# Kernel tuning notes

Hardware: AMD Instinct MI355X
Metric: run time of the kernel (lower is better)

Reference implementation:

```python
import jax, jax.numpy as jnp
import numpy as np

N, E, F, H, O, R = 50000, 600000, 128, 128, 64, 8


def setup_inputs() -> dict:
    key = jax.random.key(0)
    ks = jax.random.split(key, 10)
    x = jax.random.normal(ks[0], (N, F), dtype=jnp.float32)
    edge_index = jax.random.randint(ks[1], (2, E), 0, N, dtype=jnp.int64)
    edge_weight = jax.random.uniform(ks[2], (E,), dtype=jnp.float32)
    edge_type = jax.random.randint(ks[3], (E,), 0, R, dtype=jnp.int64)
    s = 1.0 / np.sqrt(F)
    W1 = jax.random.uniform(ks[4], (R, F, H), jnp.float32, -s, s)
    root1 = jax.random.uniform(ks[5], (F, H), jnp.float32, -s, s)
    bias1 = jnp.zeros((H,), jnp.float32)
    sh = 1.0 / np.sqrt(H)
    W2 = jax.random.uniform(ks[6], (R, H, O), jnp.float32, -sh, sh)
    root2 = jax.random.uniform(ks[7], (H, O), jnp.float32, -sh, sh)
    bias2 = jnp.zeros((O,), jnp.float32)
    return {"x": x, "edge_index": edge_index, "edge_weight": edge_weight,
            "edge_type": edge_type, "W1": W1, "root1": root1, "bias1": bias1,
            "W2": W2, "root2": root2, "bias2": bias2}


def _rgcn_conv(x, src, dst, et, ew, W, root, bias, num_nodes):
    # project every node by every relation: [N, R, out] (cheaper than per-edge
    # materialization of weight[edge_type] which is E x in x out)
    proj = jnp.einsum('nd,rdo->nro', x, W)
    # per-edge message = x_j @ W[edge_type] * edge_weight  -> [E, out]
    msg = proj[src, et] * ew[:, None]
    # weighted scatter-mean over destination nodes
    agg = jax.ops.segment_sum(msg, dst, num_segments=num_nodes)
    cnt = jax.ops.segment_sum(jnp.ones_like(ew), dst, num_segments=num_nodes)
    agg = agg / jnp.maximum(cnt, 1.0)[:, None]
    # root (self) transform + bias
    return agg + x @ root + bias


def reference(x, edge_index, edge_weight, edge_type, W1, root1, bias1, W2, root2, bias2):
    src, dst = edge_index[0], edge_index[1]
    et = edge_type.astype(jnp.int32)
    # min-max normalize edge weights as in RGCN.forward
    ew = (edge_weight - edge_weight.min()) / (edge_weight.max() - edge_weight.min() + 1e-8)
    n = x.shape[0]
    h = jax.nn.relu(_rgcn_conv(x, src, dst, et, ew, W1, root1, bias1, n))
    return _rgcn_conv(h, src, dst, et, ew, W2, root2, bias2, n)
```

## Files before the change

kernel.cpp:

```cpp
#include <hip/hip_runtime.h>

#define F_DIM 128
#define H_DIM 128
#define O_DIM 64
#define R_NUM 8

typedef __attribute__((ext_vector_type(8))) short bf16x8;
typedef __attribute__((ext_vector_type(4))) float f32x4;
typedef __attribute__((ext_vector_type(8))) unsigned short u16x8;

union V8 { bf16x8 v; short4 h[2]; };

__device__ __forceinline__ unsigned short f2b(float f) {
    unsigned u = __float_as_uint(f);
    u += 0x7FFFu + ((u >> 16) & 1u);
    return (unsigned short)(u >> 16);
}
__device__ __forceinline__ float b2f(unsigned short b) {
    return __uint_as_float(((unsigned)b) << 16);
}

__global__ __launch_bounds__(256) void setupA(
    const float* __restrict__ ew, const int* __restrict__ dst,
    const int* __restrict__ et, int E, int* __restrict__ deg2,
    float* __restrict__ bmn, float* __restrict__ bmx,
    const float* __restrict__ x, unsigned short* __restrict__ xb, long x4,
    const float* __restrict__ W1, const float* __restrict__ root1,
    const float* __restrict__ W2, const float* __restrict__ root2,
    unsigned short* __restrict__ wt1, unsigned short* __restrict__ wt2) {
    __shared__ float smn[256], smx[256];
    const int tid = threadIdx.x;
    const int gstride = gridDim.x * blockDim.x;
    int g0 = blockIdx.x * blockDim.x + tid;

    float mn = 1e30f, mx = -1e30f;
    for (int i = g0; i < E; i += gstride) {
        atomicAdd(&deg2[dst[i] * R_NUM + et[i]], 1);
        float v = ew[i];
        mn = fminf(mn, v);
        mx = fmaxf(mx, v);
    }
    smn[tid] = mn; smx[tid] = mx;
    __syncthreads();
    for (int s = 128; s > 0; s >>= 1) {
        if (tid < s) {
            smn[tid] = fminf(smn[tid], smn[tid + s]);
            smx[tid] = fmaxf(smx[tid], smx[tid + s]);
        }
        __syncthreads();
    }
    if (tid == 0) { bmn[blockIdx.x] = smn[0]; bmx[blockIdx.x] = smx[0]; }

    for (long i = g0; i < x4; i += gstride) {
        float4 v = ((const float4*)x)[i];
        ushort4 o;
        o.x = f2b(v.x); o.y = f2b(v.y); o.z = f2b(v.z); o.w = f2b(v.w);
        ((ushort4*)xb)[i] = o;
    }

    const int n1 = 9 * 128 * 128, n2 = 9 * 64 * 128;
    for (int idx = g0; idx < n1 + n2; idx += gstride) {
        if (idx < n1) {
            int r = idx / (128 * 128), rem = idx % (128 * 128);
            int n = rem / 128, k = rem % 128;
            float v = (r < 8) ? W1[((size_t)r * 128 + k) * 128 + n]
                              : root1[(size_t)k * 128 + n];
            wt1[idx] = f2b(v);
        } else {
            int j = idx - n1;
            int r = j / (64 * 128), rem = j % (64 * 128);
            int n = rem / 128, k = rem % 128;
            float v = (r < 8) ? W2[((size_t)r * 128 + k) * 64 + n]
                              : root2[(size_t)k * 64 + n];
            wt2[j] = f2b(v);
        }
    }
}

__global__ void scan1_kernel(const int* __restrict__ deg, int* __restrict__ rp,
                             int* __restrict__ bsum, float* __restrict__ invc,
                             int M, int N) {
    __shared__ int s[256];
    int base = blockIdx.x * 2048;
    int t = threadIdx.x;
    int v[8]; int loc = 0;
#pragma unroll
    for (int i = 0; i < 8; ++i) {
        int idx = base + t * 8 + i;
        v[i] = (idx < M) ? deg[idx] : 0;
        loc += v[i];
    }
    int node = blockIdx.x * 256 + t;
    if (node < N) invc[node] = 1.0f / (float)max(loc, 1);
    s[t] = loc;
    __syncthreads();
    for (int off = 1; off < 256; off <<= 1) {
        int x = (t >= off) ? s[t - off] : 0;
        __syncthreads();
        s[t] += x;
        __syncthreads();
    }
    int run = s[t] - loc;
#pragma unroll
    for (int i = 0; i < 8; ++i) {
        int idx = base + t * 8 + i;
        if (idx < M) rp[idx] = run;
        run += v[i];
    }
    if (t == 255) bsum[blockIdx.x] = s[255];
}

__global__ void scan2_mm(int* bsum, int nb, const float* __restrict__ bmn,
                         const float* __restrict__ bmx, float* mm) {
    __shared__ int s[256];
    __shared__ float smn[256], smx[256];
    int t = threadIdx.x;
    int v = (t < nb) ? bsum[t] : 0;
    s[t] = v;
    smn[t] = fminf(bmn[t], bmn[t + 256]);
    smx[t] = fmaxf(bmx[t], bmx[t + 256]);
    __syncthreads();
    for (int off = 1; off < 256; off <<= 1) {
        int x = (t >= off) ? s[t - off] : 0;
        __syncthreads();
        s[t] += x;
        __syncthreads();
    }
    if (t < nb) bsum[t] = s[t] - v;
    for (int r = 128; r > 0; r >>= 1) {
        if (t < r) {
            smn[t] = fminf(smn[t], smn[t + r]);
            smx[t] = fmaxf(smx[t], smx[t + r]);
        }
        __syncthreads();
    }
    if (t == 0) { mm[0] = smn[0]; mm[1] = smx[0]; }
}

__global__ void scan3_kernel(int* __restrict__ rp, const int* __restrict__ bsum, int M) {
    int i = blockIdx.x * blockDim.x + threadIdx.x;
    if (i < M) rp[i] += bsum[i >> 11];
}

__global__ void fill2_kernel(const int* __restrict__ src, const int* __restrict__ dst,
                             const int* __restrict__ et, const float* __restrict__ ew,
                             const float* __restrict__ mm, const float* __restrict__ invc,
                             int* __restrict__ rp2, unsigned* __restrict__ erec, int E) {
    int e = blockIdx.x * blockDim.x + threadIdx.x;
    if (e >= E) return;
    int d = dst[e];
    int pos = atomicAdd(&rp2[d * R_NUM + et[e]], 1);
    float mn = mm[0], mx = mm[1];
    unsigned wq = f2b((ew[e] - mn) / (mx - mn + 1e-8f) * invc[d]);
    erec[pos] = (wq << 17) | (unsigned)src[e];
}

__global__ __launch_bounds__(256) void gather_y(
    const int* __restrict__ rp2, const unsigned* __restrict__ erec,
    const unsigned short* __restrict__ inp,
    unsigned short* __restrict__ y, int N) {
    int gid = blockIdx.x * 256 + threadIdx.x;
    int seg = gid >> 4;
    int n = seg >> 3;
    if (n >= N) return;
    int j = (gid & 15) * 8;
    int beg = (seg == 0) ? 0 : rp2[seg - 1];
    int end = rp2[seg];
    float acc[8] = {0.f, 0.f, 0.f, 0.f, 0.f, 0.f, 0.f, 0.f};
    int k = beg;
    for (; k + 2 <= end; k += 2) {
        unsigned r0 = erec[k], r1 = erec[k + 1];
        float w0 = __uint_as_float((r0 >> 1) & 0x7FFF8000u);
        float w1 = __uint_as_float((r1 >> 1) & 0x7FFF8000u);
        u16x8 v0 = *(const u16x8*)(inp + (size_t)(r0 & 0x1FFFFu) * 128 + j);
        u16x8 v1 = *(const u16x8*)(inp + (size_t)(r1 & 0x1FFFFu) * 128 + j);
#pragma unroll
        for (int c = 0; c < 8; ++c) acc[c] += w0 * b2f(v0[c]);
#pragma unroll
        for (int c = 0; c < 8; ++c) acc[c] += w1 * b2f(v1[c]);
    }
    if (k < end) {
        unsigned r0 = erec[k];
        float w0 = __uint_as_float((r0 >> 1) & 0x7FFF8000u);
        u16x8 v0 = *(const u16x8*)(inp + (size_t)(r0 & 0x1FFFFu) * 128 + j);
#pragma unroll
        for (int c = 0; c < 8; ++c) acc[c] += w0 * b2f(v0[c]);
    }
    u16x8 o;
#pragma unroll
    for (int c = 0; c < 8; ++c) o[c] = f2b(acc[c]);
    *(u16x8*)(y + (size_t)seg * 128 + j) = o;
}

template <int NCOL, bool RELU, bool OUTB>
__global__ __launch_bounds__(256) void gemm_y(
    const unsigned short* __restrict__ y,
    const unsigned short* __restrict__ inp,
    const unsigned short* __restrict__ Wt,
    const float* __restrict__ bias,
    unsigned short* __restrict__ outb, float* __restrict__ outf, int N)
{
    constexpr int NT = NCOL / 16;
    __shared__ unsigned short smem[64 * 132 + NCOL * 132];
    unsigned short* ys  = smem;
    unsigned short* wsd = smem + 64 * 132;

    const int tid = threadIdx.x;
    const int w = tid >> 6, lane = tid & 63;
    const int quad = lane >> 4, l15 = lane & 15;
    const int n0 = blockIdx.x * 64;

    f32x4 acc[NT];
#pragma unroll
    for (int nt = 0; nt < NT; ++nt) acc[nt] = (f32x4){0.f, 0.f, 0.f, 0.f};

    for (int r = 0; r < 9; ++r) {
#pragma unroll
        for (int it = 0; it < NCOL / 16; ++it) {
            int u = tid + it * 256;
            int row = u >> 4, seg = u & 15;
            V8 v;
            v.v = *(const bf16x8*)(Wt + ((size_t)r * NCOL + row) * 128 + seg * 8);
            *(short4*)&wsd[row * 132 + seg * 8]     = v.h[0];
            *(short4*)&wsd[row * 132 + seg * 8 + 4] = v.h[1];
        }
#pragma unroll
        for (int it = 0; it < 4; ++it) {
            int u = tid + it * 256;
            int row = u >> 4, seg = u & 15;
            int node = n0 + row;
            if (node >= N) node = N - 1;
            const unsigned short* src = (r < 8)
                ? y + ((size_t)node * R_NUM + r) * 128 + seg * 8
                : inp + (size_t)node * 128 + seg * 8;
            V8 v; v.v = *(const bf16x8*)src;
            *(short4*)&ys[row * 132 + seg * 8]     = v.h[0];
            *(short4*)&ys[row * 132 + seg * 8 + 4] = v.h[1];
        }
        __syncthreads();
        const unsigned short* yrow = ys + (size_t)(w * 16 + l15) * 132 + quad * 8;
#pragma unroll
        for (int k2 = 0; k2 < 4; ++k2) {
            V8 b;
            b.h[0] = *(const short4*)(yrow + k2 * 32);
            b.h[1] = *(const short4*)(yrow + k2 * 32 + 4);
#pragma unroll
            for (int nt = 0; nt < NT; ++nt) {
                const unsigned short* ar = wsd + (size_t)(nt * 16 + l15) * 132
                                           + k2 * 32 + quad * 8;
                V8 av;
                av.h[0] = *(const short4*)ar;
                av.h[1] = *(const short4*)(ar + 4);
                acc[nt] = __builtin_amdgcn_mfma_f32_16x16x32_bf16(av.v, b.v, acc[nt], 0, 0, 0);
            }
        }
        __syncthreads();
    }

    const int gn = tid >> 2, gq = tid & 3;
    const int gnode = n0 + gn;
    if (OUTB) {
        unsigned short* stg = smem;
#pragma unroll
        for (int nt = 0; nt < NT; ++nt) {
            int c0 = nt * 16 + quad * 4;
            float4 bs = *(const float4*)(bias + c0);
            float v0 = acc[nt][0] + bs.x, v1 = acc[nt][1] + bs.y;
            float v2 = acc[nt][2] + bs.z, v3 = acc[nt][3] + bs.w;
            if (RELU) {
                v0 = fmaxf(v0, 0.f); v1 = fmaxf(v1, 0.f);
                v2 = fmaxf(v2, 0.f); v3 = fmaxf(v3, 0.f);
            }
            short4 o;
            o.x = (short)f2b(v0); o.y = (short)f2b(v1);
            o.z = (short)f2b(v2); o.w = (short)f2b(v3);
            *(short4*)&stg[(w * 16 + l15) * 136 + c0] = o;
        }
        __syncthreads();
        if (gnode < N) {
            const unsigned short* srow = stg + gn * 136 + gq * (NCOL / 4);
            unsigned short* drow = outb + (size_t)gnode * NCOL + gq * (NCOL / 4);
#pragma unroll
            for (int c = 0; c < NCOL / 32; ++c)
                *(bf16x8*)(drow + c * 8) = *(const bf16x8*)(srow + c * 8);
        }
    } else {
        float* stg = (float*)smem;
#pragma unroll
        for (int nt = 0; nt < NT; ++nt) {
            int c0 = nt * 16 + quad * 4;
            float4 bs = *(const float4*)(bias + c0);
            float v0 = acc[nt][0] + bs.x, v1 = acc[nt][1] + bs.y;
            float v2 = acc[nt][2] + bs.z, v3 = acc[nt][3] + bs.w;
            if (RELU) {
                v0 = fmaxf(v0, 0.f); v1 = fmaxf(v1, 0.f);
                v2 = fmaxf(v2, 0.f); v3 = fmaxf(v3, 0.f);
            }
            *(float4*)&stg[(w * 16 + l15) * 68 + c0] = make_float4(v0, v1, v2, v3);
        }
        __syncthreads();
        if (gnode < N) {
            const float* srow = stg + gn * 68 + gq * (NCOL / 4);
            float* drow = outf + (size_t)gnode * NCOL + gq * (NCOL / 4);
#pragma unroll
            for (int c = 0; c < NCOL / 16; ++c)
                *(float4*)(drow + c * 4) = *(const float4*)(srow + c * 4);
        }
    }
}

extern "C" void kernel_launch(void* const* d_in, const int* in_sizes, int n_in,
                              void* d_out, int out_size, void* d_ws, size_t ws_size,
                              hipStream_t stream) {
    const float* x     = (const float*)d_in[0];
    const int*   ei    = (const int*)d_in[1];
    const float* ew    = (const float*)d_in[2];
    const int*   et    = (const int*)d_in[3];
    const float* W1    = (const float*)d_in[4];
    const float* root1 = (const float*)d_in[5];
    const float* bias1 = (const float*)d_in[6];
    const float* W2    = (const float*)d_in[7];
    const float* root2 = (const float*)d_in[8];
    const float* bias2 = (const float*)d_in[9];

    const int N = in_sizes[0] / F_DIM;
    const int E = in_sizes[2];
    const int M2 = N * R_NUM;
    const int* srcp = ei;
    const int* dstp = ei + E;

    int* base = (int*)d_ws;
    float* mm    = (float*)base;
    float* invc  = (float*)(base + 16);
    int*   deg2  = base + 16 + N;
    int*   rp2   = deg2 + M2;
    int*   bsum  = rp2 + M2;
    float* bmn   = (float*)(bsum + 256);
    float* bmx   = bmn + 512;
    unsigned* erec = (unsigned*)(bmx + 512);
    unsigned short* xb  = (unsigned short*)(erec + E);
    unsigned short* hb  = xb + (size_t)N * 128;
    unsigned short* wt1 = hb + (size_t)N * 128;
    unsigned short* wt2 = wt1 + 9 * 128 * 128;
    unsigned short* y   = wt2 + 9 * 64 * 128;

    const int TB = 256;
    int blocksE = (E + TB - 1) / TB;
    int nb = (M2 + 2047) / 2048;
    long x4 = (long)N * 128 / 4;

    hipMemsetAsync(deg2, 0, (size_t)M2 * sizeof(int), stream);
    setupA<<<512, TB, 0, stream>>>(ew, dstp, et, E, deg2, bmn, bmx,
                                   x, xb, x4, W1, root1, W2, root2, wt1, wt2);
    scan1_kernel<<<nb, TB, 0, stream>>>(deg2, rp2, bsum, invc, M2, N);
    scan2_mm<<<1, TB, 0, stream>>>(bsum, nb, bmn, bmx, mm);
    scan3_kernel<<<(M2 + TB - 1) / TB, TB, 0, stream>>>(rp2, bsum, M2);
    fill2_kernel<<<blocksE, TB, 0, stream>>>(srcp, dstp, et, ew, mm, invc,
                                             rp2, erec, E);

    int gatB = (int)(((long)M2 * 16 + TB - 1) / TB);
    int gB = (N + 63) / 64;

    gather_y<<<gatB, TB, 0, stream>>>(rp2, erec, xb, y, N);
    gemm_y<H_DIM, true, true><<<gB, TB, 0, stream>>>(y, xb, wt1, bias1, hb, nullptr, N);
    gather_y<<<gatB, TB, 0, stream>>>(rp2, erec, hb, y, N);
    gemm_y<O_DIM, false, false><<<gB, TB, 0, stream>>>(y, hb, wt2, bias2, nullptr,
                                                       (float*)d_out, N);
}
```

Baseline: 317.5 us.

## Double-buffer Y tiles and keep weight fragments in registers in gemm_y

Rewrites the gemm_y inner loop so each wave owns a slice of output columns and loads its weight fragments directly from global memory into registers, dropping the per-relation LDS staging of the weight matrix. Y tiles are double-buffered in LDS, with the next relation's tile prefetched into registers during the MFMAs, leaving one barrier per iteration instead of two. This aims to overlap global loads with compute and cut LDS traffic and syncs, at the cost of more VGPRs for weight fragments and uncoalesced-ish global weight reads, which may lower occupancy.

Result: slower. 325.3 us (+2.5%).

```diff
diff --git a/kernel.cpp b/kernel.cpp
--- a/kernel.cpp
+++ b/kernel.cpp
@@ -200,58 +200,79 @@
     const float* __restrict__ bias,
     unsigned short* __restrict__ outb, float* __restrict__ outf, int N)
 {
-    constexpr int NT = NCOL / 16;
-    __shared__ unsigned short smem[64 * 132 + NCOL * 132];
-    unsigned short* ys  = smem;
-    unsigned short* wsd = smem + 64 * 132;
+    constexpr int NTW = NCOL / 64;
+    __shared__ unsigned short ybuf[2][64 * 132];
 
     const int tid = threadIdx.x;
     const int w = tid >> 6, lane = tid & 63;
     const int quad = lane >> 4, l15 = lane & 15;
     const int n0 = blockIdx.x * 64;
 
-    f32x4 acc[NT];
-#pragma unroll
-    for (int nt = 0; nt < NT; ++nt) acc[nt] = (f32x4){0.f, 0.f, 0.f, 0.f};
+    const int srow = tid >> 4;
+    const int sseg = tid & 15;
+
+    f32x4 acc[4][NTW];
+#pragma unroll
+    for (int m = 0; m < 4; ++m)
+#pragma unroll
+        for (int nt = 0; nt < NTW; ++nt) acc[m][nt] = (f32x4){0.f, 0.f, 0.f, 0.f};
+
+#pragma unroll
+    for (int it = 0; it < 4; ++it) {
+        int row = srow + it * 16;
+        int node = n0 + row;
+        if (node >= N) node = N - 1;
+        V8 v;
+        v.v = *(const bf16x8*)(y + ((size_t)node * R_NUM + 0) * 128 + sseg * 8);
+        *(short4*)&ybuf[0][row * 132 + sseg * 8]     = v.h[0];
+        *(short4*)&ybuf[0][row * 132 + sseg * 8 + 4] = v.h[1];
+    }
+    __syncthreads();
 
     for (int r = 0; r < 9; ++r) {
-#pragma unroll
-        for (int it = 0; it < NCOL / 16; ++it) {
-            int u = tid + it * 256;
-            int row = u >> 4, seg = u & 15;
-            V8 v;
-            v.v = *(const bf16x8*)(Wt + ((size_t)r * NCOL + row) * 128 + seg * 8);
-            *(short4*)&wsd[row * 132 + seg * 8]     = v.h[0];
-            *(short4*)&wsd[row * 132 + seg * 8 + 4] = v.h[1];
-        }
-#pragma unroll
-        for (int it = 0; it < 4; ++it) {
-            int u = tid + it * 256;
-            int row = u >> 4, seg = u & 15;
-            int node = n0 + row;
-            if (node >= N) node = N - 1;
-            const unsigned short* src = (r < 8)
-                ? y + ((size_t)node * R_NUM + r) * 128 + seg * 8
-                : inp + (size_t)node * 128 + seg * 8;
-            V8 v; v.v = *(const bf16x8*)src;
-            *(short4*)&ys[row * 132 + seg * 8]     = v.h[0];
-            *(short4*)&ys[row * 132 + seg * 8 + 4] = v.h[1];
-        }
-        __syncthreads();
-        const unsigned short* yrow = ys + (size_t)(w * 16 + l15) * 132 + quad * 8;
-#pragma unroll
-        for (int k2 = 0; k2 < 4; ++k2) {
-            V8 b;
-            b.h[0] = *(const short4*)(yrow + k2 * 32);
-            b.h[1] = *(const short4*)(yrow + k2 * 32 + 4);
-#pragma unroll
-            for (int nt = 0; nt < NT; ++nt) {
-                const unsigned short* ar = wsd + (size_t)(nt * 16 + l15) * 132
-                                           + k2 * 32 + quad * 8;
-                V8 av;
-                av.h[0] = *(const short4*)ar;
-                av.h[1] = *(const short4*)(ar + 4);
-                acc[nt] = __builtin_amdgcn_mfma_f32_16x16x32_bf16(av.v, b.v, acc[nt], 0, 0, 0);
+        const int buf = r & 1;
+        V8 pre[4];
+        if (r < 8) {
+            const int rn = r + 1;
+#pragma unroll
+            for (int it = 0; it < 4; ++it) {
+                int row = srow + it * 16;
+                int node = n0 + row;
+                if (node >= N) node = N - 1;
+                const unsigned short* src = (rn < 8)
+                    ? y + ((size_t)node * R_NUM + rn) * 128 + sseg * 8
+                    : inp + (size_t)node * 128 + sseg * 8;
+                pre[it].v = *(const bf16x8*)src;
+            }
+        }
+        bf16x8 afr[NTW][4];
+#pragma unroll
+        for (int nt = 0; nt < NTW; ++nt)
+#pragma unroll
+            for (int k2 = 0; k2 < 4; ++k2)
+                afr[nt][k2] = *(const bf16x8*)(
+                    Wt + ((size_t)r * NCOL + (w * NTW + nt) * 16 + l15) * 128
+                       + k2 * 32 + quad * 8);
+#pragma unroll
+        for (int m = 0; m < 4; ++m) {
+            const unsigned short* yrow = &ybuf[buf][(m * 16 + l15) * 132 + quad * 8];
+#pragma unroll
+            for (int k2 = 0; k2 < 4; ++k2) {
+                V8 b;
+                b.h[0] = *(const short4*)(yrow + k2 * 32);
+                b.h[1] = *(const short4*)(yrow + k2 * 32 + 4);
+#pragma unroll
+                for (int nt = 0; nt < NTW; ++nt)
+                    acc[m][nt] = __builtin_amdgcn_mfma_f32_16x16x32_bf16(
+                        afr[nt][k2], b.v, acc[m][nt], 0, 0, 0);
+            }
+        }
+        if (r < 8) {
+#pragma unroll
+            for (int it = 0; it < 4; ++it) {
+                int row = srow + it * 16;
+                *(short4*)&ybuf[buf ^ 1][row * 132 + sseg * 8]     = pre[it].h[0];
+                *(short4*)&ybuf[buf ^ 1][row * 132 + sseg * 8 + 4] = pre[it].h[1];
             }
         }
         __syncthreads();
@@ -260,51 +281,57 @@
     const int gn = tid >> 2, gq = tid & 3;
     const int gnode = n0 + gn;
     if (OUTB) {
-        unsigned short* stg = smem;
-#pragma unroll
-        for (int nt = 0; nt < NT; ++nt) {
-            int c0 = nt * 16 + quad * 4;
-            float4 bs = *(const float4*)(bias + c0);
-            float v0 = acc[nt][0] + bs.x, v1 = acc[nt][1] + bs.y;
-            float v2 = acc[nt][2] + bs.z, v3 = acc[nt][3] + bs.w;
-            if (RELU) {
-                v0 = fmaxf(v0, 0.f); v1 = fmaxf(v1, 0.f);
-                v2 = fmaxf(v2, 0.f); v3 = fmaxf(v3, 0.f);
-            }
-            short4 o;
-            o.x = (short)f2b(v0); o.y = (short)f2b(v1);
-            o.z = (short)f2b(v2); o.w = (short)f2b(v3);
-            *(short4*)&stg[(w * 16 + l15) * 136 + c0] = o;
-        }
+        unsigned short* stg = &ybuf[0][0];
+#pragma unroll
+        for (int m = 0; m < 4; ++m)
+#pragma unroll
+            for (int nt = 0; nt < NTW; ++nt) {
+                int node_l = m * 16 + l15;
+                int c0 = (w * NTW + nt) * 16 + quad * 4;
+                float4 bs = *(const float4*)(bias + c0);
+                float v0 = acc[m][nt][0] + bs.x, v1 = acc[m][nt][1] + bs.y;
+                float v2 = acc[m][nt][2] + bs.z, v3 = acc[m][nt][3] + bs.w;
+                if (RELU) {
+                    v0 = fmaxf(v0, 0.f); v1 = fmaxf(v1, 0.f);
+                    v2 = fmaxf(v2, 0.f); v3 = fmaxf(v3, 0.f);
+                }
+                short4 o;
+                o.x = (short)f2b(v0); o.y = (short)f2b(v1);
+                o.z = (short)f2b(v2); o.w = (short)f2b(v3);
+                *(short4*)&stg[node_l * 136 + c0] = o;
+            }
         __syncthreads();
         if (gnode < N) {
-            const unsigned short* srow = stg + gn * 136 + gq * (NCOL / 4);
+            const unsigned short* srw = stg + gn * 136 + gq * (NCOL / 4);
             unsigned short* drow = outb + (size_t)gnode * NCOL + gq * (NCOL / 4);
 #pragma unroll
             for (int c = 0; c < NCOL / 32; ++c)
-                *(bf16x8*)(drow + c * 8) = *(const bf16x8*)(srow + c * 8);
+                *(bf16x8*)(drow + c * 8) = *(const bf16x8*)(srw + c * 8);
         }
     } else {
-        float* stg = (float*)smem;
-#pragma unroll
-        for (int nt = 0; nt < NT; ++nt) {
-            int c0 = nt * 16 + quad * 4;
-            float4 bs = *(const float4*)(bias + c0);
-            float v0 = acc[nt][0] + bs.x, v1 = acc[nt][1] + bs.y;
-            float v2 = acc[nt][2] + bs.z, v3 = acc[nt][3] + bs.w;
-            if (RELU) {
-                v0 = fmaxf(v0, 0.f); v1 = fmaxf(v1, 0.f);
-                v2 = fmaxf(v2, 0.f); v3 = fmaxf(v3, 0.f);
-            }
-            *(float4*)&stg[(w * 16 + l15) * 68 + c0] = make_float4(v0, v1, v2, v3);
-        }
+        float* stg = (float*)&ybuf[0][0];
+#pragma unroll
+        for (int m = 0; m < 4; ++m)
+#pragma unroll
+            for (int nt = 0; nt < NTW; ++nt) {
+                int node_l = m * 16 + l15;
+                int c0 = (w * NTW + nt) * 16 + quad * 4;
+                float4 bs = *(const float4*)(bias + c0);
+                float v0 = acc[m][nt][0] + bs.x, v1 = acc[m][nt][1] + bs.y;
+                float v2 = acc[m][nt][2] + bs.z, v3 = acc[m][nt][3] + bs.w;
+                if (RELU) {
+                    v0 = fmaxf(v0, 0.f); v1 = fmaxf(v1, 0.f);
+                    v2 = fmaxf(v2, 0.f); v3 = fmaxf(v3, 0.f);
+                }
+                *(float4*)&stg[node_l * 68 + c0] = make_float4(v0, v1, v2, v3);
+            }
         __syncthreads();
         if (gnode < N) {
-            const float* srow = stg + gn * 68 + gq * (NCOL / 4);
+            const float* srw = stg + gn * 68 + gq * (NCOL / 4);
             float* drow = outf + (size_t)gnode * NCOL + gq * (NCOL / 4);
 #pragma unroll
             for (int c = 0; c < NCOL / 16; ++c)
-                *(float4*)(drow + c * 4) = *(const float4*)(srow + c * 4);
+                *(float4*)(drow + c * 4) = *(const float4*)(srw + c * 4);
         }
     }
 }
```

## Project layer-2 features before aggregation and fold scan offsets into consumers

Applied to the files above, without the earlier changes.

Layer 2 now projects every node by every relation (and root) into a 64-wide bf16 buffer first, then gathers the projected rows per destination node. Because the output width is 64 rather than 128, this halves the bytes moved in the second edge gather, and it drops the separate aggregate-then-GEMM path for that layer. It also removes the scan3 pass by adding the block prefix sums inside fill2 and the gather kernels. The cost is a larger intermediate (9×N×64) and a per-relation serial loop in the final gather.

New measurement: 298.2 us. 1.06x faster.

```diff
diff --git a/kernel.cpp b/kernel.cpp
--- a/kernel.cpp
+++ b/kernel.cpp
@@ -137,26 +137,24 @@
     if (t == 0) { mm[0] = smn[0]; mm[1] = smx[0]; }
 }
 
-__global__ void scan3_kernel(int* __restrict__ rp, const int* __restrict__ bsum, int M) {
-    int i = blockIdx.x * blockDim.x + threadIdx.x;
-    if (i < M) rp[i] += bsum[i >> 11];
-}
-
 __global__ void fill2_kernel(const int* __restrict__ src, const int* __restrict__ dst,
                              const int* __restrict__ et, const float* __restrict__ ew,
                              const float* __restrict__ mm, const float* __restrict__ invc,
-                             int* __restrict__ rp2, unsigned* __restrict__ erec, int E) {
+                             int* __restrict__ rp2, const int* __restrict__ bsum,
+                             unsigned* __restrict__ erec, int E) {
     int e = blockIdx.x * blockDim.x + threadIdx.x;
     if (e >= E) return;
     int d = dst[e];
-    int pos = atomicAdd(&rp2[d * R_NUM + et[e]], 1);
+    int i = d * R_NUM + et[e];
+    int pos = atomicAdd(&rp2[i], 1) + bsum[i >> 11];
     float mn = mm[0], mx = mm[1];
     unsigned wq = f2b((ew[e] - mn) / (mx - mn + 1e-8f) * invc[d]);
     erec[pos] = (wq << 17) | (unsigned)src[e];
 }
 
 __global__ __launch_bounds__(256) void gather_y(
-    const int* __restrict__ rp2, const unsigned* __restrict__ erec,
+    const int* __restrict__ rp2, const int* __restrict__ bsum,
+    const unsigned* __restrict__ erec,
     const unsigned short* __restrict__ inp,
     unsigned short* __restrict__ y, int N) {
     int gid = blockIdx.x * 256 + threadIdx.x;
@@ -164,8 +162,8 @@
     int n = seg >> 3;
     if (n >= N) return;
     int j = (gid & 15) * 8;
-    int beg = (seg == 0) ? 0 : rp2[seg - 1];
-    int end = rp2[seg];
+    int beg = (seg == 0) ? 0 : rp2[seg - 1] + bsum[(seg - 1) >> 11];
+    int end = rp2[seg] + bsum[seg >> 11];
     float acc[8] = {0.f, 0.f, 0.f, 0.f, 0.f, 0.f, 0.f, 0.f};
     int k = beg;
     for (; k + 2 <= end; k += 2) {
@@ -192,13 +190,13 @@
     *(u16x8*)(y + (size_t)seg * 128 + j) = o;
 }
 
-template <int NCOL, bool RELU, bool OUTB>
+template <int NCOL, bool RELU>
 __global__ __launch_bounds__(256) void gemm_y(
     const unsigned short* __restrict__ y,
     const unsigned short* __restrict__ inp,
     const unsigned short* __restrict__ Wt,
     const float* __restrict__ bias,
-    unsigned short* __restrict__ outb, float* __restrict__ outf, int N)
+    unsigned short* __restrict__ outb, int N)
 {
     constexpr int NT = NCOL / 16;
     __shared__ unsigned short smem[64 * 132 + NCOL * 132];
@@ -259,54 +257,156 @@
 
     const int gn = tid >> 2, gq = tid & 3;
     const int gnode = n0 + gn;
-    if (OUTB) {
-        unsigned short* stg = smem;
-#pragma unroll
-        for (int nt = 0; nt < NT; ++nt) {
+    unsigned short* stg = smem;
+#pragma unroll
+    for (int nt = 0; nt < NT; ++nt) {
+        int c0 = nt * 16 + quad * 4;
+        float4 bs = *(const float4*)(bias + c0);
+        float v0 = acc[nt][0] + bs.x, v1 = acc[nt][1] + bs.y;
+        float v2 = acc[nt][2] + bs.z, v3 = acc[nt][3] + bs.w;
+        if (RELU) {
+            v0 = fmaxf(v0, 0.f); v1 = fmaxf(v1, 0.f);
+            v2 = fmaxf(v2, 0.f); v3 = fmaxf(v3, 0.f);
+        }
+        short4 o;
+        o.x = (short)f2b(v0); o.y = (short)f2b(v1);
+        o.z = (short)f2b(v2); o.w = (short)f2b(v3);
+        *(short4*)&stg[(w * 16 + l15) * 136 + c0] = o;
+    }
+    __syncthreads();
+    if (gnode < N) {
+        const unsigned short* srw = stg + gn * 136 + gq * (NCOL / 4);
+        unsigned short* drow = outb + (size_t)gnode * NCOL + gq * (NCOL / 4);
+#pragma unroll
+        for (int c = 0; c < NCOL / 32; ++c)
+            *(bf16x8*)(drow + c * 8) = *(const bf16x8*)(srw + c * 8);
+    }
+}
+
+__global__ __launch_bounds__(256) void gemm_proj2(
+    const unsigned short* __restrict__ h,
+    const unsigned short* __restrict__ Wt,
+    unsigned short* __restrict__ proj2,
+    int N)
+{
+    __shared__ unsigned short hs[64 * 132];
+    __shared__ unsigned short wsd[64 * 132];
+    __shared__ unsigned short ts[64 * 68];
+
+    const int tid = threadIdx.x;
+    const int w = tid >> 6, lane = tid & 63;
+    const int quad = lane >> 4, l15 = lane & 15;
+    const int n0 = blockIdx.x * 64;
+
+#pragma unroll
+    for (int it = 0; it < 4; ++it) {
+        int u = tid + it * 256;
+        int row = u >> 4, seg = u & 15;
+        int node = n0 + row;
+        if (node >= N) node = N - 1;
+        V8 v; v.v = *(const bf16x8*)(h + (size_t)node * 128 + seg * 8);
+        *(short4*)&hs[row * 132 + seg * 8]     = v.h[0];
+        *(short4*)&hs[row * 132 + seg * 8 + 4] = v.h[1];
+    }
+
+    for (int r = 0; r < 9; ++r) {
+#pragma unroll
+        for (int it = 0; it < 4; ++it) {
+            int u = tid + it * 256;
+            int row = u >> 4, seg = u & 15;
+            V8 v;
+            v.v = *(const bf16x8*)(Wt + ((size_t)r * 64 + row) * 128 + seg * 8);
+            *(short4*)&wsd[row * 132 + seg * 8]     = v.h[0];
+            *(short4*)&wsd[row * 132 + seg * 8 + 4] = v.h[1];
+        }
+        __syncthreads();
+        f32x4 acc[4];
+#pragma unroll
+        for (int nt = 0; nt < 4; ++nt) acc[nt] = (f32x4){0.f, 0.f, 0.f, 0.f};
+        const unsigned short* yrow = hs + (size_t)(w * 16 + l15) * 132 + quad * 8;
+#pragma unroll
+        for (int k2 = 0; k2 < 4; ++k2) {
+            V8 b;
+            b.h[0] = *(const short4*)(yrow + k2 * 32);
+            b.h[1] = *(const short4*)(yrow + k2 * 32 + 4);
+#pragma unroll
+            for (int nt = 0; nt < 4; ++nt) {
+                const unsigned short* ar = wsd + (size_t)(nt * 16 + l15) * 132
+                                           + k2 * 32 + quad * 8;
+                V8 av;
+                av.h[0] = *(const short4*)ar;
+                av.h[1] = *(const short4*)(ar + 4);
+                acc[nt] = __builtin_amdgcn_mfma_f32_16x16x32_bf16(av.v, b.v, acc[nt], 0, 0, 0);
+            }
+        }
+        unsigned short* tw = ts + w * 16 * 68;
+#pragma unroll
+        for (int nt = 0; nt < 4; ++nt) {
             int c0 = nt * 16 + quad * 4;
-            float4 bs = *(const float4*)(bias + c0);
-            float v0 = acc[nt][0] + bs.x, v1 = acc[nt][1] + bs.y;
-            float v2 = acc[nt][2] + bs.z, v3 = acc[nt][3] + bs.w;
-            if (RELU) {
-                v0 = fmaxf(v0, 0.f); v1 = fmaxf(v1, 0.f);
-                v2 = fmaxf(v2, 0.f); v3 = fmaxf(v3, 0.f);
-            }
             short4 o;
-            o.x = (short)f2b(v0); o.y = (short)f2b(v1);
-            o.z = (short)f2b(v2); o.w = (short)f2b(v3);
-            *(short4*)&stg[(w * 16 + l15) * 136 + c0] = o;
-        }
-        __syncthreads();
-        if (gnode < N) {
-            const unsigned short* srow = stg + gn * 136 + gq * (NCOL / 4);
-            unsigned short* drow = outb + (size_t)gnode * NCOL + gq * (NCOL / 4);
-#pragma unroll
-            for (int c = 0; c < NCOL / 32; ++c)
-                *(bf16x8*)(drow + c * 8) = *(const bf16x8*)(srow + c * 8);
-        }
-    } else {
-        float* stg = (float*)smem;
-#pragma unroll
-        for (int nt = 0; nt < NT; ++nt) {
-            int c0 = nt * 16 + quad * 4;
-            float4 bs = *(const float4*)(bias + c0);
-            float v0 = acc[nt][0] + bs.x, v1 = acc[nt][1] + bs.y;
-            float v2 = acc[nt][2] + bs.z, v3 = acc[nt][3] + bs.w;
-            if (RELU) {
-                v0 = fmaxf(v0, 0.f); v1 = fmaxf(v1, 0.f);
-                v2 = fmaxf(v2, 0.f); v3 = fmaxf(v3, 0.f);
-            }
-            *(float4*)&stg[(w * 16 + l15) * 68 + c0] = make_float4(v0, v1, v2, v3);
-        }
-        __syncthreads();
-        if (gnode < N) {
-            const float* srow = stg + gn * 68 + gq * (NCOL / 4);
-            float* drow = outf + (size_t)gnode * NCOL + gq * (NCOL / 4);
-#pragma unroll
-            for (int c = 0; c < NCOL / 16; ++c)
-                *(float4*)(drow + c * 4) = *(const float4*)(srow + c * 4);
-        }
-    }
+            o.x = (short)f2b(acc[nt][0]); o.y = (short)f2b(acc[nt][1]);
+            o.z = (short)f2b(acc[nt][2]); o.w = (short)f2b(acc[nt][3]);
+            *(short4*)&tw[l15 * 68 + c0] = o;
+        }
+#pragma unroll
+        for (int jj = 0; jj < 2; ++jj) {
+            int rl = (lane >> 3) + 8 * jj;
+            int off = (lane & 7) * 8;
+            int g = n0 + w * 16 + rl;
+            V8 v;
+            v.h[0] = *(const short4*)&tw[rl * 68 + off];
+            v.h[1] = *(const short4*)&tw[rl * 68 + off + 4];
+            if (g < N)
+                *(bf16x8*)(proj2 + ((size_t)r * N + g) * 64 + off) = v.v;
+        }
+        __syncthreads();
+    }
+}
+
+__global__ __launch_bounds__(256) void gather_out2(
+    const int* __restrict__ rp2, const int* __restrict__ bsum,
+    const unsigned* __restrict__ erec,
+    const unsigned short* __restrict__ proj2,
+    const float* __restrict__ bias,
+    float* __restrict__ out, int N)
+{
+    int gid = blockIdx.x * 256 + threadIdx.x;
+    int n = gid >> 3;
+    if (n >= N) return;
+    int j = (gid & 7) * 8;
+
+    int base = n * R_NUM;
+    int bs_n = bsum[base >> 11];
+    int4 ea = *(const int4*)(rp2 + base);
+    int4 eb = *(const int4*)(rp2 + base + 4);
+    int ends[8] = {ea.x + bs_n, ea.y + bs_n, ea.z + bs_n, ea.w + bs_n,
+                   eb.x + bs_n, eb.y + bs_n, eb.z + bs_n, eb.w + bs_n};
+    int k = (n == 0) ? 0 : rp2[base - 1] + bsum[(base - 1) >> 11];
+
+    float acc[8] = {0.f, 0.f, 0.f, 0.f, 0.f, 0.f, 0.f, 0.f};
+#pragma unroll
+    for (int r = 0; r < 8; ++r) {
+        int end = ends[r];
+        for (; k < end; ++k) {
+            unsigned rec = erec[k];
+            float wgt = __uint_as_float((rec >> 1) & 0x7FFF8000u);
+            u16x8 v = *(const u16x8*)(proj2 + ((size_t)r * N + (rec & 0x1FFFFu)) * 64 + j);
+#pragma unroll
+            for (int c = 0; c < 8; ++c) acc[c] += wgt * b2f(v[c]);
+        }
+    }
+    u16x8 sv = *(const u16x8*)(proj2 + ((size_t)8 * N + n) * 64 + j);
+    float4 b0 = *(const float4*)(bias + j);
+    float4 b1 = *(const float4*)(bias + j + 4);
+    float* o = out + (size_t)n * 64 + j;
+    o[0] = acc[0] + b2f(sv[0]) + b0.x;
+    o[1] = acc[1] + b2f(sv[1]) + b0.y;
+    o[2] = acc[2] + b2f(sv[2]) + b0.z;
+    o[3] = acc[3] + b2f(sv[3]) + b0.w;
+    o[4] = acc[4] + b2f(sv[4]) + b1.x;
+    o[5] = acc[5] + b2f(sv[5]) + b1.y;
+    o[6] = acc[6] + b2f(sv[6]) + b1.z;
+    o[7] = acc[7] + b2f(sv[7]) + b1.w;
 }
 
 extern "C" void kernel_launch(void* const* d_in, const int* in_sizes, int n_in,
@@ -343,6 +443,7 @@
     unsigned short* wt1 = hb + (size_t)N * 128;
     unsigned short* wt2 = wt1 + 9 * 128 * 128;
     unsigned short* y   = wt2 + 9 * 64 * 128;
+    unsigned short* proj2 = y;
 
     const int TB = 256;
     int blocksE = (E + TB - 1) / TB;
@@ -354,16 +455,17 @@
                                    x, xb, x4, W1, root1, W2, root2, wt1, wt2);
     scan1_kernel<<<nb, TB, 0, stream>>>(deg2, rp2, bsum, invc, M2, N);
     scan2_mm<<<1, TB, 0, stream>>>(bsum, nb, bmn, bmx, mm);
-    scan3_kernel<<<(M2 + TB - 1) / TB, TB, 0, stream>>>(rp2, bsum, M2);
     fill2_kernel<<<blocksE, TB, 0, stream>>>(srcp, dstp, et, ew, mm, invc,
-                                             rp2, erec, E);
+                                             rp2, bsum, erec, E);
 
     int gatB = (int)(((long)M2 * 16 + TB - 1) / TB);
     int gB = (N + 63) / 64;
 
-    gather_y<<<gatB, TB, 0, stream>>>(rp2, erec, xb, y, N);
-    gemm_y<H_DIM, true, true><<<gB, TB, 0, stream>>>(y, xb, wt1, bias1, hb, nullptr, N);
-    gather_y<<<gatB, TB, 0, stream>>>(rp2, erec, hb, y, N);
-    gemm_y<O_DIM, false, false><<<gB, TB, 0, stream>>>(y, hb, wt2, bias2, nullptr,
-                                                       (float*)d_out, N);
-}
+    gather_y<<<gatB, TB, 0, stream>>>(rp2, bsum, erec, xb, y, N);
+    gemm_y<H_DIM, true><<<gB, TB, 0, stream>>>(y, xb, wt1, bias1, hb, N);
+
+    gemm_proj2<<<gB, TB, 0, stream>>>(hb, wt2, proj2, N);
+    int g2B = (int)(((long)N * 8 + TB - 1) / TB);
+    gather_out2<<<g2B, TB, 0, stream>>>(rp2, bsum, erec, proj2, bias2,
+                                        (float*)d_out, N);
+}
```
